# Kernel tuning notes

Measured on AMD Instinct MI355X. Metric: run time of the kernel, lower is better.

The kernel has to match this reference:

```python
import math
import jax, jax.numpy as jnp
from jax import lax
import numpy as np

PATCHES = [(8, 8), (4, 4), (2, 2), (1, 1)]  # (width, height) per scale
BN_EPS = 1e-5


def setup_inputs() -> dict:
    key = jax.random.key(0)
    ks = jax.random.split(key, 9)
    b, d, h, w = 4, 256, 64, 64
    s = 1.0 / math.sqrt(d)
    return {
        "x": jax.random.normal(ks[0], (b, d, h, w), jnp.float32),
        "wq": jax.random.normal(ks[1], (d, d), jnp.float32) * s,
        "bq": jax.random.normal(ks[2], (d,), jnp.float32) * 0.02,
        "wk": jax.random.normal(ks[3], (d, d), jnp.float32) * s,
        "bk": jax.random.normal(ks[4], (d,), jnp.float32) * 0.02,
        "wv": jax.random.normal(ks[5], (d, d), jnp.float32) * s,
        "bv": jax.random.normal(ks[6], (d,), jnp.float32) * 0.02,
        "w_out": jax.random.normal(ks[7], (d, d, 3, 3), jnp.float32) * (s / 3.0),
        "b_out": jax.random.normal(ks[8], (d,), jnp.float32) * 0.02,
        "gamma": jnp.ones((d,), jnp.float32),
        "beta": jnp.zeros((d,), jnp.float32),
    }


def _to_tokens(t, b, dk, out_h, ph, out_w, pw):
    # [b, dk, h, w] -> [b, out_h*out_w, dk*ph*pw]
    t = t.reshape(b, dk, out_h, ph, out_w, pw)
    t = t.transpose(0, 2, 4, 1, 3, 5)
    return t.reshape(b, out_h * out_w, dk * ph * pw)


def reference(x, wq, bq, wk, bk, wv, bv, w_out, b_out, gamma, beta):
    b, c, h, w = x.shape
    # 1x1 conv projections == channel matmuls
    q = jnp.einsum('bchw,oc->bohw', x, wq) + bq[None, :, None, None]
    k = jnp.einsum('bchw,oc->bohw', x, wk) + bk[None, :, None, None]
    v = jnp.einsum('bchw,oc->bohw', x, wv) + bv[None, :, None, None]

    dk = c // len(PATCHES)
    outs = []
    for i, (pw, ph) in enumerate(PATCHES):
        sl = slice(i * dk, (i + 1) * dk)
        out_h, out_w = h // ph, w // pw
        Q = _to_tokens(q[:, sl], b, dk, out_h, ph, out_w, pw)
        K = _to_tokens(k[:, sl], b, dk, out_h, ph, out_w, pw)
        V = _to_tokens(v[:, sl], b, dk, out_h, ph, out_w, pw)
        scores = jnp.einsum('bnd,bmd->bnm', Q, K) / math.sqrt(Q.shape[-1])
        p = jax.nn.softmax(scores, axis=-1)
        y = jnp.einsum('bnm,bmd->bnd', p, V)
        # tokens -> [b, dk, h, w]
        y = y.reshape(b, out_h, out_w, dk, ph, pw)
        y = y.transpose(0, 3, 1, 4, 2, 5).reshape(b, dk, h, w)
        outs.append(y)
    out = jnp.concatenate(outs, axis=1)

    # 3x3 conv, padding=1
    z = lax.conv_general_dilated(out, w_out, (1, 1), 'SAME',
                                 dimension_numbers=('NCHW', 'OIHW', 'NCHW'))
    z = z + b_out[None, :, None, None]
    # BatchNorm2d (training-mode batch stats)
    mean = jnp.mean(z, axis=(0, 2, 3), keepdims=True)
    var = jnp.var(z, axis=(0, 2, 3), keepdims=True)
    zn = (z - mean) * lax.rsqrt(var + BN_EPS)
    zn = zn * gamma[None, :, None, None] + beta[None, :, None, None]
    # LeakyReLU(0.2)
    return jnp.where(zn > 0, zn, 0.2 * zn)
```

## Files before the change

kernel.cpp:

```cpp
#include <hip/hip_runtime.h>
#include <cmath>


#define OFF_XB  0LL
#define OFF_QB  2097152LL
#define OFF_SS  8388608LL
#define OFF_PP  12582912LL
#define OFF_YT  14680064LL
#define OFF_WQK 18874368LL
#define OFF_BIA 18972672LL
#define OFF_WCV 18973440LL
#define OFF_STT 19268352LL
#define OFF_SP0 19268864LL
#define OFF_S1  19399936LL
#define OFF_P0  19662080LL
#define OFF_P1  19670272LL
#define OFF_LI  19801344LL

#define FC 0.18033688f
#define CSHIFT 6.0f

typedef __attribute__((ext_vector_type(8))) short short8;
typedef __attribute__((ext_vector_type(4))) float f32x4;

__device__ inline unsigned short f2bf(float f) {
  unsigned u = __float_as_uint(f);
  u += 0x7fff + ((u >> 16) & 1);
  return (unsigned short)(u >> 16);
}

__device__ inline unsigned cvt_pk_bf16(float a, float b) {
  unsigned r;
  asm("v_cvt_pk_bf16_f32 %0, %1, %2" : "=v"(r) : "v"(a), "v"(b));
  return r;
}

__global__ __launch_bounds__(256) void prep_k(
    const float* __restrict__ x, unsigned short* __restrict__ xb,
    const float* __restrict__ wq, const float* __restrict__ wk,
    const float* __restrict__ wv, const float* __restrict__ bq,
    const float* __restrict__ bk, const float* __restrict__ bv,
    unsigned short* __restrict__ Wqkv, float* __restrict__ biasQKV,
    const float* __restrict__ wcv, unsigned short* __restrict__ Wcb)
{
  const int bid = blockIdx.x, t = threadIdx.x;
  if (bid < 256) {
    __shared__ unsigned short rowb[256][66];
    const int b = bid >> 6, y = bid & 63;
    for (int i = t; i < 16384; i += 256) {
      int c = i >> 6, xx = i & 63;
      rowb[c][xx] = f2bf(x[((long long)(b*256 + c) << 12) + (y << 6) + xx]);
    }
    __syncthreads();
    unsigned int* outw = (unsigned int*)(xb + ((long long)bid << 14));
    for (int i = t; i < 8192; i += 256) {
      int xx = i >> 7, c2 = (i & 127) * 2;
      outw[xx*128 + (c2 >> 1)] = (unsigned)rowb[c2][xx]
                               | ((unsigned)rowb[c2+1][xx] << 16);
    }
  } else if (bid < 1024) {
    const int row = bid - 256;
    const int which = row >> 8, oc = row & 255;
    const float* src = which == 0 ? wq : which == 1 ? wk : wv;
    Wqkv[row*256 + t] = f2bf(src[oc*256 + t]);
    if (row < 3) {
      const float* bs = row == 0 ? bq : row == 1 ? bk : bv;
      biasQKV[row*256 + t] = bs[t];
    }
  } else {
    int i = (bid - 1024)*256 + t;
    int tap = i >> 16, oc = (i >> 8) & 255, ic = i & 255;
    Wcb[i] = f2bf(wcv[((long long)(oc*256 + ic))*9 + tap]);
  }
}

template<int EPI, int SH = 0>
__device__ void gemm_nt_body(
    const unsigned short* __restrict__ A, const unsigned short* __restrict__ B,
    void* __restrict__ Cv, const float* __restrict__ bias,
    int M, int N, int K, int lda, int ldb, int ldc,
    long long sA, long long sB, long long sC, float alpha,
    int bx, int by, int bz)
{
  const int t = threadIdx.x, l = t & 63;
  const int lr = l & 15, lg = l >> 4;
  const int w = t >> 6, wm = w >> 1, wn = w & 1;
  const int m0 = by*128 + wm*64, n0 = bx*128 + wn*64;
  if (m0 >= M || n0 >= N) return;
  const unsigned short* Ab = A + (long long)bz*sA + (long long)(m0 + lr)*lda + lg*8;
  const unsigned short* Bb = B + (long long)bz*sB + (long long)(n0 + lr)*ldb + lg*8;

  f32x4 acc[4][4] = {};
#pragma unroll 2
  for (int kk = 0; kk < K; kk += 32) {
    short8 af[4], bf[4];
#pragma unroll
    for (int i = 0; i < 4; i++)
      af[i] = *(const short8*)(Ab + (long long)i*16*lda + kk);
#pragma unroll
    for (int i = 0; i < 4; i++)
      bf[i] = *(const short8*)(Bb + (long long)i*16*ldb + kk);
#pragma unroll
    for (int mf = 0; mf < 4; mf++)
#pragma unroll
      for (int nf = 0; nf < 4; nf++)
        acc[mf][nf] = __builtin_amdgcn_mfma_f32_16x16x32_bf16(
            af[mf], bf[nf], acc[mf][nf], 0, 0, 0);
  }

  if (EPI == 0) {
    float* C = (float*)Cv + (long long)bz*sC;
#pragma unroll
    for (int mf = 0; mf < 4; mf++)
#pragma unroll
      for (int r = 0; r < 4; r++) {
        const int row = m0 + mf*16 + lg*4 + r;
#pragma unroll
        for (int nf = 0; nf < 4; nf++)
          C[(long long)row*ldc + n0 + nf*16 + lr] = acc[mf][nf][r] * alpha;
      }
  } else if (EPI == 1) {
    unsigned short* Qbase = (unsigned short*)Cv;
#pragma unroll
    for (int mf = 0; mf < 4; mf++)
#pragma unroll
      for (int r = 0; r < 4; r++) {
        const int gi = m0 + mf*16 + lg*4 + r;
        const int which = gi >> 8, ch = gi & 255;
        const int scale = ch >> 6, c = ch & 63;
        const int sh = 3 - scale, msk = (1 << sh) - 1;
        const bool tr = (which == 2);
        const float bb = bias[gi];
        unsigned short* dst = Qbase + (long long)which*4194304
                            + (long long)scale*1048576 + (long long)bz*262144;
#pragma unroll
        for (int nf = 0; nf < 4; nf++) {
          const int gj = n0 + nf*16 + lr;
          const int y = gj >> 6, xx = gj & 63;
          const int n = (y >> sh)*(64 >> sh) + (xx >> sh);
          const int d = (c << (2*sh)) + ((y & msk) << sh) + (xx & msk);
          const long long idx = tr
              ? (long long)d*(4096 >> (2*sh)) + n
              : (long long)n*(64 << (2*sh)) + d;
          dst[idx] = f2bf(acc[mf][nf][r] + bb);
        }
      }
  } else {
    unsigned short* inb = (unsigned short*)Cv;
    constexpr int msk = (1 << SH) - 1;
    constexpr int scale = 3 - SH;
#pragma unroll
    for (int mf = 0; mf < 4; mf++)
#pragma unroll
      for (int r = 0; r < 4; r++) {
        const int gi = m0 + mf*16 + lg*4 + r;
        const int ty = gi >> (6 - SH), tx = gi & ((64 >> SH) - 1);
#pragma unroll
        for (int nf = 0; nf < 4; nf++) {
          const int gj = n0 + nf*16 + lr;
          const int c = gj >> (2*SH);
          const int y = (ty << SH) | ((gj >> SH) & msk);
          const int x = (tx << SH) | (gj & msk);
          inb[((((long long)bz << 12) + (y << 6) + x) << 8) + scale*64 + c]
              = f2bf(acc[mf][nf][r]);
        }
      }
  }
}

__global__ __launch_bounds__(256) void qkv_k(
    const unsigned short* __restrict__ Wqkv, const unsigned short* __restrict__ xb,
    unsigned short* __restrict__ Qu, const float* __restrict__ biasQKV)
{
  gemm_nt_body<1>(Wqkv, xb, (void*)Qu, biasQKV, 768, 4096, 256, 256, 256, 0,
                  0, 1048576, 0, 1.0f, blockIdx.x, blockIdx.y, blockIdx.z);
}

__device__ void s0_scores_wave(
    const unsigned short* __restrict__ Q, const unsigned short* __restrict__ K,
    float* __restrict__ Sp, int bid)
{
  const int t = threadIdx.x, l = t & 63, w = t >> 6;
  const int lr = l & 15, lg = l >> 4;
  const int task = bid*4 + w;
  const int b = task >> 3, ks = task & 7;
  const unsigned short* Qb = Q + (long long)b*262144;
  const unsigned short* Kb = K + (long long)b*262144;
  f32x4 acc[4][4] = {};
  const int k0 = ks*512;
#pragma unroll 2
  for (int kk = k0; kk < k0 + 512; kk += 32) {
    short8 af[4], bf[4];
#pragma unroll
    for (int i = 0; i < 4; i++)
      af[i] = *(const short8*)(Qb + (long long)(i*16 + lr)*4096 + kk + lg*8);
#pragma unroll
    for (int i = 0; i < 4; i++)
      bf[i] = *(const short8*)(Kb + (long long)(i*16 + lr)*4096 + kk + lg*8);
#pragma unroll
    for (int mf = 0; mf < 4; mf++)
#pragma unroll
      for (int nf = 0; nf < 4; nf++)
        acc[mf][nf] = __builtin_amdgcn_mfma_f32_16x16x32_bf16(
            af[mf], bf[nf], acc[mf][nf], 0, 0, 0);
  }
#pragma unroll
  for (int mf = 0; mf < 4; mf++)
#pragma unroll
    for (int r = 0; r < 4; r++) {
      const int row = mf*16 + lg*4 + r;
#pragma unroll
      for (int nf = 0; nf < 4; nf++)
        Sp[(((long long)(ks*4 + b)*64 + row) << 6) + nf*16 + lr]
            = acc[mf][nf][r];
    }
}

__device__ void flash3_body(
    const unsigned short* __restrict__ Q3, const unsigned short* __restrict__ K3,
    const unsigned short* __restrict__ Vt3, float* __restrict__ part,
    float* __restrict__ lig, int bx, int b, int sp)
{
  constexpr int LD = 72;
  __shared__ unsigned short KVs[2][2][64*LD];
  __shared__ unsigned short Ps[64*LD];
  const int t = threadIdx.x, l = t & 63, w = t >> 6;
  const int lr = l & 15, lg = l >> 4;
  const int q0 = bx * 64;
  const long long base = (long long)b * 262144;
  const unsigned short* Qg = Q3 + base;
  const unsigned short* Kg = K3 + base;
  const unsigned short* Vg = Vt3 + base;

  short8 bq[2];
  bq[0] = *(const short8*)(Qg + (long long)(q0 + w*16 + lr)*64 + lg*8);
  bq[1] = *(const short8*)(Qg + (long long)(q0 + w*16 + lr)*64 + 32 + lg*8);

  f32x4 acc[4] = {};
  float li = 0.f;

  const int r_ = t >> 3, c8_ = (t & 7) * 8;
  uint4 kreg[2], vreg[2];

#define LOADKV(KT) do { \
    const int k0_ = (KT) * 64; \
    _Pragma("unroll") \
    for (int it = 0; it < 2; it++) { \
      const int rr = r_ + it*32; \
      kreg[it] = *(const uint4*)(Kg + (long long)(k0_ + rr)*64 + c8_); \
      vreg[it] = *(const uint4*)(Vg + (long long)rr*4096 + k0_ + c8_); \
    } } while (0)
#define STOREKV(BUF) do { \
    _Pragma("unroll") \
    for (int it = 0; it < 2; it++) { \
      const int rr = r_ + it*32; \
      *(uint4*)(KVs[BUF][0] + rr*LD + c8_) = kreg[it]; \
      *(uint4*)(KVs[BUF][1] + rr*LD + c8_) = vreg[it]; \
    } } while (0)

  const int kt0 = sp * 16;
  LOADKV(kt0);
  STOREKV(0);
  __syncthreads();

  for (int i = 0; i < 16; ++i) {
    const int kt = kt0 + i;
    if (i < 15) LOADKV(kt + 1);
    const unsigned short* Ksb = KVs[i & 1][0];
    const unsigned short* Vsb = KVs[i & 1][1];
    f32x4 s[4];
#pragma unroll
    for (int cf = 0; cf < 4; cf++) {
      short8 ak0 = *(const short8*)(Ksb + (cf*16 + lr)*LD + lg*8);
      short8 ak1 = *(const short8*)(Ksb + (cf*16 + lr)*LD + 32 + lg*8);
      f32x4 zz = {};
      zz = __builtin_amdgcn_mfma_f32_16x16x32_bf16(ak0, bq[0], zz, 0,0,0);
      s[cf] = __builtin_amdgcn_mfma_f32_16x16x32_bf16(ak1, bq[1], zz, 0,0,0);
    }
    float p[16], psum = 0.f;
#pragma unroll
    for (int cf = 0; cf < 4; cf++)
#pragma unroll
      for (int r = 0; r < 4; r++) {
        float e = exp2f(fmaf(s[cf][r], FC, -CSHIFT));
        p[cf*4 + r] = e; psum += e;
      }
    li += psum;
    {
      unsigned short* pr = Ps + (w*16 + lr)*LD;
#pragma unroll
      for (int cf = 0; cf < 4; cf++) {
        *(unsigned*)(pr + cf*16 + lg*4)     = cvt_pk_bf16(p[cf*4+0], p[cf*4+1]);
        *(unsigned*)(pr + cf*16 + lg*4 + 2) = cvt_pk_bf16(p[cf*4+2], p[cf*4+3]);
      }
    }
    short8 bp0 = *(const short8*)(Ps + (w*16 + lr)*LD + lg*8);
    short8 bp1 = *(const short8*)(Ps + (w*16 + lr)*LD + 32 + lg*8);
#pragma unroll
    for (int df = 0; df < 4; df++) {
      short8 av0 = *(const short8*)(Vsb + (df*16 + lr)*LD + lg*8);
      short8 av1 = *(const short8*)(Vsb + (df*16 + lr)*LD + 32 + lg*8);
      acc[df] = __builtin_amdgcn_mfma_f32_16x16x32_bf16(av0, bp0, acc[df], 0,0,0);
      acc[df] = __builtin_amdgcn_mfma_f32_16x16x32_bf16(av1, bp1, acc[df], 0,0,0);
    }
    if (i < 15) {
      STOREKV((i + 1) & 1);
      __syncthreads();
    }
  }
#undef LOADKV
#undef STOREKV
  li += __shfl_xor(li, 16);
  li += __shfl_xor(li, 32);
  const long long prow = (long long)(sp*4 + b)*4096 + q0 + w*16 + lr;
#pragma unroll
  for (int df = 0; df < 4; df++)
    *(float4*)(part + prow*64 + df*16 + lg*4) =
        make_float4(acc[df][0], acc[df][1], acc[df][2], acc[df][3]);
  if (lg == 0) lig[prow] = li;
}

__global__ __launch_bounds__(256) void stageA_k(
    const unsigned short* __restrict__ Qu, const unsigned short* __restrict__ Ku,
    const unsigned short* __restrict__ Vu,
    float* __restrict__ Sp0, float* __restrict__ S1, float* __restrict__ S2,
    float* __restrict__ part, float* __restrict__ lig)
{
  const int bid = blockIdx.x;
  if (bid < 1024) {
    flash3_body(Qu+3145728, Ku+3145728, Vu+3145728, part, lig,
                bid & 63, (bid >> 6) & 3, bid >> 8);
  } else if (bid < 1032) {
    s0_scores_wave(Qu, Ku, Sp0, bid - 1024);
  } else if (bid < 1048) {
    int q = bid - 1032;
    gemm_nt_body<0>(Qu+1048576, Ku+1048576, (void*)S1, nullptr,
        256, 256, 1024, 1024, 1024, 256, 262144, 262144, 65536, 0.03125f,
        q & 1, (q >> 1) & 1, q >> 2);
  } else {
    int q = bid - 1048;
    gemm_nt_body<0>(Qu+2097152, Ku+2097152, (void*)S2, nullptr,
        1024, 1024, 256, 256, 256, 1024, 262144, 262144, 1048576, 0.0625f,
        q & 7, (q >> 3) & 7, q >> 6);
  }
}

template<int CNT>
__device__ void softmax_row(const float* __restrict__ S,
                            unsigned short* __restrict__ P, long long row)
{
  const int l = threadIdx.x & 63;
  const float* p = S + row*(CNT*64);
  unsigned short* o = P + row*(CNT*64);
  float v[CNT];
  float mx = -1e30f;
#pragma unroll
  for (int i = 0; i < CNT; i++) { v[i] = p[i*64 + l]; mx = fmaxf(mx, v[i]); }
#pragma unroll
  for (int off = 1; off < 64; off <<= 1) mx = fmaxf(mx, __shfl_xor(mx, off, 64));
  float sum = 0.f;
#pragma unroll
  for (int i = 0; i < CNT; i++) { v[i] = __expf(v[i] - mx); sum += v[i]; }
#pragma unroll
  for (int off = 1; off < 64; off <<= 1) sum += __shfl_xor(sum, off, 64);
  const float inv = 1.f / sum;
#pragma unroll
  for (int i = 0; i < CNT; i++) o[i*64 + l] = f2bf(v[i] * inv);
}

__global__ __launch_bounds__(256) void stageB_k(
    const float* __restrict__ Sp0, unsigned short* __restrict__ P0,
    const float* __restrict__ S1, unsigned short* __restrict__ P1,
    const float* __restrict__ S2, unsigned short* __restrict__ P2,
    const float* __restrict__ part, const float* __restrict__ lig,
    unsigned short* __restrict__ inb)
{
  const int bid = blockIdx.x, t = threadIdx.x, l = t & 63, w = t >> 6;
  if (bid < 1024) {
    softmax_row<16>(S2, P2, (long long)bid*4 + w);
  } else if (bid < 1280) {
    softmax_row<4>(S1, P1, (long long)(bid - 1024)*4 + w);
  } else if (bid < 1344) {
    const int row = (bid - 1280)*4 + w;
    const int b = row >> 6, r = row & 63;
    float v = 0.f;
#pragma unroll
    for (int ks = 0; ks < 8; ks++)
      v += Sp0[(((long long)(ks*4 + b)*64 + r) << 6) + l];
    v *= 0.015625f;
    float mx = v;
#pragma unroll
    for (int off = 1; off < 64; off <<= 1) mx = fmaxf(mx, __shfl_xor(mx, off, 64));
    float e = __expf(v - mx), sum = e;
#pragma unroll
    for (int off = 1; off < 64; off <<= 1) sum += __shfl_xor(sum, off, 64);
    P0[(row << 6) + l] = f2bf(e / sum);
  } else {
    const long long row = (long long)(bid - 1344)*64 + (t >> 2);
    const int dd = (t & 3) * 16;
    float L = 0.f;
#pragma unroll
    for (int s = 0; s < 4; s++) L += lig[(long long)s*16384 + row];
    const float inv = 1.f / L;
#pragma unroll
    for (int j = 0; j < 4; j++) {
      float ax = 0.f, ay = 0.f, az = 0.f, aw = 0.f;
#pragma unroll
      for (int s = 0; s < 4; s++) {
        float4 v = *(const float4*)(part + ((long long)s*16384 + row)*64 + dd + j*4);
        ax += v.x; ay += v.y; az += v.z; aw += v.w;
      }
      ushort4 ov;
      ov.x = f2bf(ax*inv); ov.y = f2bf(ay*inv);
      ov.z = f2bf(az*inv); ov.w = f2bf(aw*inv);
      *(ushort4*)(inb + row*256 + 192 + dd + j*4) = ov;
    }
  }
}

__global__ __launch_bounds__(256) void stageC_k(
    const unsigned short* __restrict__ P0, const unsigned short* __restrict__ P1,
    const unsigned short* __restrict__ P2, const unsigned short* __restrict__ Vu,
    unsigned short* __restrict__ inb)
{
  const int bid = blockIdx.x;
  if (bid < 128) {
    int q = bid;
    gemm_nt_body<2,3>(P0, Vu, (void*)inb, nullptr,
        64, 4096, 64, 64, 64, 0, 4096, 262144, 0, 1.0f,
        q & 31, 0, q >> 5);
  } else if (bid < 192) {
    int q = bid - 128;
    gemm_nt_body<2,2>(P1, Vu+1048576, (void*)inb, nullptr,
        256, 1024, 256, 256, 256, 0, 65536, 262144, 0, 1.0f,
        q & 7, (q >> 3) & 1, q >> 4);
  } else {
    int q = bid - 192;
    gemm_nt_body<2,1>(P2, Vu+2097152, (void*)inb, nullptr,
        1024, 256, 1024, 1024, 1024, 0, 1048576, 262144, 0, 1.0f,
        q & 1, (q >> 1) & 7, q >> 4);
  }
}

__global__ __launch_bounds__(512) void conv_mfma_k(
    const unsigned short* __restrict__ inb, const unsigned short* __restrict__ Wb,
    const float* __restrict__ bias, float* __restrict__ z)
{
  __shared__ unsigned short lds[2][6*66*32];
  const int t = threadIdx.x;
  const int l = t & 63, wid = t >> 6;
  const int lr = l & 15, lg = l >> 4;
  const int waveM = wid >> 2, waveN = wid & 3;
  const int b = blockIdx.x >> 4, y0 = (blockIdx.x & 15) * 4;
  const int oc0 = blockIdx.y * 64 + waveM * 32;
  const long long inbase = (long long)b * 1048576;
  const int kgrp = lg * 8;

  f32x4 acc[2][4] = {};
  uint4 sreg[4];

#define CLOAD(IC0) do { \
    _Pragma("unroll") \
    for (int i = 0; i < 4; i++) { \
      int q = t + i*512; \
      if (q < 1584) { \
        int ic8 = q & 3, cc = (q >> 2) % 66, rr = q / 264; \
        int gy = y0 - 1 + rr, gx = cc - 1; \
        uint4 v = make_uint4(0u,0u,0u,0u); \
        if ((unsigned)gy < 64u && (unsigned)gx < 64u) \
          v = *(const uint4*)(inb + inbase + ((long long)(gy*64+gx))*256 \
                              + (IC0) + ic8*8); \
        sreg[i] = v; \
      } \
    } } while (0)
#define CSTORE(BUF) do { \
    _Pragma("unroll") \
    for (int i = 0; i < 4; i++) { \
      int q = t + i*512; \
      if (q < 1584) *(uint4*)(&lds[BUF][q*8]) = sreg[i]; \
    } } while (0)

  CLOAD(0);
  CSTORE(0);
  __syncthreads();

  for (int c = 0; c < 8; ++c) {
    const int ic0 = c * 32;
    if (c < 7) CLOAD(ic0 + 32);
    const unsigned short* wbase = Wb + (long long)(oc0 + lr)*256 + ic0 + kgrp;
    short8 afr[9][2];
#pragma unroll
    for (int tap = 0; tap < 9; tap++) {
      afr[tap][0] = *(const short8*)(wbase + (long long)tap*65536);
      afr[tap][1] = *(const short8*)(wbase + (long long)tap*65536 + 16*256);
    }
    const unsigned short* L = lds[c & 1];
#pragma unroll
    for (int ky = 0; ky < 3; ky++) {
#pragma unroll
      for (int kx = 0; kx < 3; kx++) {
        const int tap = ky*3 + kx;
#pragma unroll
        for (int nf = 0; nf < 4; nf++) {
          int pix = waveN*64 + nf*16 + lr;
          int rp = pix >> 6, xx = pix & 63;
          short8 bf = *(const short8*)(L + ((rp + ky)*66 + xx + kx)*32 + kgrp);
          acc[0][nf] = __builtin_amdgcn_mfma_f32_16x16x32_bf16(
              afr[tap][0], bf, acc[0][nf], 0, 0, 0);
          acc[1][nf] = __builtin_amdgcn_mfma_f32_16x16x32_bf16(
              afr[tap][1], bf, acc[1][nf], 0, 0, 0);
        }
      }
    }
    if (c < 7) {
      CSTORE((c + 1) & 1);
      __syncthreads();
    }
  }
#undef CLOAD
#undef CSTORE

  const long long zb = ((long long)b * 256) << 12;
#pragma unroll
  for (int mf = 0; mf < 2; mf++) {
#pragma unroll
    for (int r = 0; r < 4; r++) {
      const int oc = oc0 + mf*16 + lg*4 + r;
      const float bb = bias[oc];
      const long long rowbase = zb + ((long long)oc << 12) + y0*64;
#pragma unroll
      for (int nf = 0; nf < 4; nf++) {
        int pix = waveN*64 + nf*16 + lr;
        z[rowbase + pix] = acc[mf][nf][r] + bb;
      }
    }
  }
}

__global__ __launch_bounds__(256) void bn_stats_k(
    const float* __restrict__ z, float* __restrict__ stats)
{
  const int ch = blockIdx.x, t = threadIdx.x;
  float s = 0.f, q = 0.f;
  for (int b = 0; b < 4; b++) {
    const float* p = z + ((long long)(b*256 + ch) << 12);
    for (int i = t; i < 4096; i += 256) { float v = p[i]; s += v; q += v*v; }
  }
  __shared__ float rs[256], rq[256];
  rs[t] = s; rq[t] = q; __syncthreads();
  for (int st = 128; st > 0; st >>= 1) {
    if (t < st) { rs[t] += rs[t+st]; rq[t] += rq[t+st]; }
    __syncthreads();
  }
  if (t == 0) {
    float mean = rs[0] * (1.f/16384.f);
    float var  = rq[0] * (1.f/16384.f) - mean*mean;
    stats[ch]       = mean;
    stats[256 + ch] = rsqrtf(var + 1e-5f);
  }
}

__global__ __launch_bounds__(256) void bn_apply_k(
    const float* __restrict__ z, const float* __restrict__ stats,
    const float* __restrict__ gamma, const float* __restrict__ beta,
    float* __restrict__ out)
{
  long long i4 = ((long long)blockIdx.x*256 + threadIdx.x) * 4;
  int ch = (int)((i4 >> 12) & 255);
  float mean = stats[ch], rsg = stats[256 + ch];
  float g = gamma[ch], bt = beta[ch];
  float4 v = *(const float4*)(z + i4);
  float r[4] = {v.x, v.y, v.z, v.w};
#pragma unroll
  for (int j = 0; j < 4; j++) {
    float u = (r[j] - mean) * rsg * g + bt;
    r[j] = u > 0.f ? u : 0.2f * u;
  }
  *(float4*)(out + i4) = make_float4(r[0], r[1], r[2], r[3]);
}

extern "C" void kernel_launch(void* const* d_in, const int* in_sizes, int n_in,
                              void* d_out, int out_size, void* d_ws, size_t ws_size,
                              hipStream_t stream)
{
  const float* x     = (const float*)d_in[0];
  const float* wq    = (const float*)d_in[1];
  const float* bq    = (const float*)d_in[2];
  const float* wk    = (const float*)d_in[3];
  const float* bk    = (const float*)d_in[4];
  const float* wv    = (const float*)d_in[5];
  const float* bv    = (const float*)d_in[6];
  const float* w_out = (const float*)d_in[7];
  const float* b_out = (const float*)d_in[8];
  const float* gamma = (const float*)d_in[9];
  const float* beta  = (const float*)d_in[10];
  float* out = (float*)d_out;

  float* ws = (float*)d_ws;
  unsigned short* xb  = (unsigned short*)(ws + OFF_XB);
  unsigned short* Qu  = (unsigned short*)(ws + OFF_QB);
  unsigned short* Ku  = Qu + 4194304;
  unsigned short* Vu  = Qu + 8388608;
  float* S2  = ws + OFF_SS;
  unsigned short* P2 = (unsigned short*)(ws + OFF_PP);
  float* part = ws + OFF_YT;
  unsigned short* Wqk = (unsigned short*)(ws + OFF_WQK);
  float* biasQ = ws + OFF_BIA;
  unsigned short* Wcv = (unsigned short*)(ws + OFF_WCV);
  float* St  = ws + OFF_STT;
  float* Sp0 = ws + OFF_SP0;
  float* S1  = ws + OFF_S1;
  unsigned short* P0 = (unsigned short*)(ws + OFF_P0);
  unsigned short* P1 = (unsigned short*)(ws + OFF_P1);
  float* lig = ws + OFF_LI;
  unsigned short* inb = (unsigned short*)(ws + OFF_XB);
  float* z = ws + OFF_YT;

  dim3 blk(256);

  prep_k<<<dim3(3328), blk, 0, stream>>>(
      x, xb, wq, wk, wv, bq, bk, bv, Wqk, biasQ, w_out, Wcv);

  qkv_k<<<dim3(32,6,4), blk, 0, stream>>>(Wqk, xb, Qu, biasQ);

  stageA_k<<<dim3(1304), blk, 0, stream>>>(Qu, Ku, Vu, Sp0, S1, S2, part, lig);

  stageB_k<<<dim3(1600), blk, 0, stream>>>(
      Sp0, P0, S1, P1, S2, P2, part, lig, inb);

  stageC_k<<<dim3(256), blk, 0, stream>>>(P0, P1, P2, Vu, inb);

  conv_mfma_k<<<dim3(64,4), dim3(512), 0, stream>>>(inb, Wcv, b_out, z);

  bn_stats_k<<<dim3(256), blk, 0, stream>>>(z, St);
  bn_apply_k<<<dim3(4096), blk, 0, stream>>>(z, St, gamma, beta, out);
}
```

Measured before the change: 246.8 us.

## Reorder stageA blocks, single-buffer flash KV, vectorize softmax and BN stats

Several unrelated changes. The flash attention body drops register-prefetched double buffering of K/V in favour of a single shared buffer loaded synchronously each tile, which cuts LDS use and register pressure and may raise occupancy, but it loses load/compute overlap. StageA now schedules the small score GEMM blocks before the flash blocks. Softmax rows and BN statistics switch to float4 loads with packed bf16 stores, which changes each lane's element mapping to contiguous chunks.

Measured after the change: 225.8 us. 8.5% less time.

```diff
diff --git a/kernel.cpp b/kernel.cpp
--- a/kernel.cpp
+++ b/kernel.cpp
@@ -222,7 +222,8 @@
     float* __restrict__ lig, int bx, int b, int sp)
 {
   constexpr int LD = 72;
-  __shared__ unsigned short KVs[2][2][64*LD];
+  __shared__ unsigned short Ks[64*LD];
+  __shared__ unsigned short Vs[64*LD];
   __shared__ unsigned short Ps[64*LD];
   const int t = threadIdx.x, l = t & 63, w = t >> 6;
   const int lr = l & 15, lg = l >> 4;
@@ -240,39 +241,23 @@
   float li = 0.f;
 
   const int r_ = t >> 3, c8_ = (t & 7) * 8;
-  uint4 kreg[2], vreg[2];
-
-#define LOADKV(KT) do { \
-    const int k0_ = (KT) * 64; \
-    _Pragma("unroll") \
-    for (int it = 0; it < 2; it++) { \
-      const int rr = r_ + it*32; \
-      kreg[it] = *(const uint4*)(Kg + (long long)(k0_ + rr)*64 + c8_); \
-      vreg[it] = *(const uint4*)(Vg + (long long)rr*4096 + k0_ + c8_); \
-    } } while (0)
-#define STOREKV(BUF) do { \
-    _Pragma("unroll") \
-    for (int it = 0; it < 2; it++) { \
-      const int rr = r_ + it*32; \
-      *(uint4*)(KVs[BUF][0] + rr*LD + c8_) = kreg[it]; \
-      *(uint4*)(KVs[BUF][1] + rr*LD + c8_) = vreg[it]; \
-    } } while (0)
-
-  const int kt0 = sp * 16;
-  LOADKV(kt0);
-  STOREKV(0);
-  __syncthreads();
-
-  for (int i = 0; i < 16; ++i) {
-    const int kt = kt0 + i;
-    if (i < 15) LOADKV(kt + 1);
-    const unsigned short* Ksb = KVs[i & 1][0];
-    const unsigned short* Vsb = KVs[i & 1][1];
+  for (int kt = sp*16; kt < sp*16 + 16; kt++) {
+    const int k0 = kt * 64;
+    __syncthreads();
+#pragma unroll
+    for (int it = 0; it < 2; it++) {
+      const int rr = r_ + it*32;
+      *(uint4*)(Ks + rr*LD + c8_) =
+          *(const uint4*)(Kg + (long long)(k0 + rr)*64 + c8_);
+      *(uint4*)(Vs + rr*LD + c8_) =
+          *(const uint4*)(Vg + (long long)rr*4096 + k0 + c8_);
+    }
+    __syncthreads();
     f32x4 s[4];
 #pragma unroll
     for (int cf = 0; cf < 4; cf++) {
-      short8 ak0 = *(const short8*)(Ksb + (cf*16 + lr)*LD + lg*8);
-      short8 ak1 = *(const short8*)(Ksb + (cf*16 + lr)*LD + 32 + lg*8);
+      short8 ak0 = *(const short8*)(Ks + (cf*16 + lr)*LD + lg*8);
+      short8 ak1 = *(const short8*)(Ks + (cf*16 + lr)*LD + 32 + lg*8);
       f32x4 zz = {};
       zz = __builtin_amdgcn_mfma_f32_16x16x32_bf16(ak0, bq[0], zz, 0,0,0);
       s[cf] = __builtin_amdgcn_mfma_f32_16x16x32_bf16(ak1, bq[1], zz, 0,0,0);
@@ -298,18 +283,12 @@
     short8 bp1 = *(const short8*)(Ps + (w*16 + lr)*LD + 32 + lg*8);
 #pragma unroll
     for (int df = 0; df < 4; df++) {
-      short8 av0 = *(const short8*)(Vsb + (df*16 + lr)*LD + lg*8);
-      short8 av1 = *(const short8*)(Vsb + (df*16 + lr)*LD + 32 + lg*8);
+      short8 av0 = *(const short8*)(Vs + (df*16 + lr)*LD + lg*8);
+      short8 av1 = *(const short8*)(Vs + (df*16 + lr)*LD + 32 + lg*8);
       acc[df] = __builtin_amdgcn_mfma_f32_16x16x32_bf16(av0, bp0, acc[df], 0,0,0);
       acc[df] = __builtin_amdgcn_mfma_f32_16x16x32_bf16(av1, bp1, acc[df], 0,0,0);
     }
-    if (i < 15) {
-      STOREKV((i + 1) & 1);
-      __syncthreads();
-    }
-  }
-#undef LOADKV
-#undef STOREKV
+  }
   li += __shfl_xor(li, 16);
   li += __shfl_xor(li, 32);
   const long long prow = (long long)(sp*4 + b)*4096 + q0 + w*16 + lr;
@@ -327,21 +306,22 @@
     float* __restrict__ part, float* __restrict__ lig)
 {
   const int bid = blockIdx.x;
-  if (bid < 1024) {
-    flash3_body(Qu+3145728, Ku+3145728, Vu+3145728, part, lig,
-                bid & 63, (bid >> 6) & 3, bid >> 8);
-  } else if (bid < 1032) {
-    s0_scores_wave(Qu, Ku, Sp0, bid - 1024);
-  } else if (bid < 1048) {
-    int q = bid - 1032;
+  if (bid < 8) {
+    s0_scores_wave(Qu, Ku, Sp0, bid);
+  } else if (bid < 24) {
+    int q = bid - 8;
     gemm_nt_body<0>(Qu+1048576, Ku+1048576, (void*)S1, nullptr,
         256, 256, 1024, 1024, 1024, 256, 262144, 262144, 65536, 0.03125f,
         q & 1, (q >> 1) & 1, q >> 2);
-  } else {
-    int q = bid - 1048;
+  } else if (bid < 280) {
+    int q = bid - 24;
     gemm_nt_body<0>(Qu+2097152, Ku+2097152, (void*)S2, nullptr,
         1024, 1024, 256, 256, 256, 1024, 262144, 262144, 1048576, 0.0625f,
         q & 7, (q >> 3) & 7, q >> 6);
+  } else {
+    const int f = bid - 280;
+    flash3_body(Qu+3145728, Ku+3145728, Vu+3145728, part, lig,
+                f & 63, (f >> 6) & 3, f >> 8);
   }
 }
 
@@ -350,12 +330,17 @@
                             unsigned short* __restrict__ P, long long row)
 {
   const int l = threadIdx.x & 63;
-  const float* p = S + row*(CNT*64);
-  unsigned short* o = P + row*(CNT*64);
+  const float* p = S + row*(CNT*64) + l*CNT;
+  unsigned short* o = P + row*(CNT*64) + l*CNT;
   float v[CNT];
-  float mx = -1e30f;
-#pragma unroll
-  for (int i = 0; i < CNT; i++) { v[i] = p[i*64 + l]; mx = fmaxf(mx, v[i]); }
+#pragma unroll
+  for (int i = 0; i < CNT; i += 4) {
+    float4 f = *(const float4*)(p + i);
+    v[i] = f.x; v[i+1] = f.y; v[i+2] = f.z; v[i+3] = f.w;
+  }
+  float mx = v[0];
+#pragma unroll
+  for (int i = 1; i < CNT; i++) mx = fmaxf(mx, v[i]);
 #pragma unroll
   for (int off = 1; off < 64; off <<= 1) mx = fmaxf(mx, __shfl_xor(mx, off, 64));
   float sum = 0.f;
@@ -365,7 +350,11 @@
   for (int off = 1; off < 64; off <<= 1) sum += __shfl_xor(sum, off, 64);
   const float inv = 1.f / sum;
 #pragma unroll
-  for (int i = 0; i < CNT; i++) o[i*64 + l] = f2bf(v[i] * inv);
+  for (int i = 0; i < CNT; i += 4) {
+    unsigned w0 = cvt_pk_bf16(v[i]*inv,   v[i+1]*inv);
+    unsigned w1 = cvt_pk_bf16(v[i+2]*inv, v[i+3]*inv);
+    *(uint2*)(o + i) = make_uint2(w0, w1);
+  }
 }
 
 __global__ __launch_bounds__(256) void stageB_k(
@@ -543,8 +532,12 @@
   const int ch = blockIdx.x, t = threadIdx.x;
   float s = 0.f, q = 0.f;
   for (int b = 0; b < 4; b++) {
-    const float* p = z + ((long long)(b*256 + ch) << 12);
-    for (int i = t; i < 4096; i += 256) { float v = p[i]; s += v; q += v*v; }
+    const float4* p = (const float4*)(z + ((long long)(b*256 + ch) << 12));
+    for (int i = t; i < 1024; i += 256) {
+      float4 v = p[i];
+      s += v.x + v.y + v.z + v.w;
+      q += v.x*v.x + v.y*v.y + v.z*v.z + v.w*v.w;
+    }
   }
   __shared__ float rs[256], rq[256];
   rs[t] = s; rq[t] = q; __syncthreads();
```
